# Kernel optimization log

Measured on AMD Instinct MI355X. Metric: run time of the kernel, lower is better.

The kernel has to match this reference:

```python
import jax, jax.numpy as jnp
import numpy as np

B = 16          # events per minibatch
P = 4096        # generated points per event
Q = 4096        # ground-truth points per event
SPATIAL_SIZE = 256.0


def setup_inputs() -> dict:
    key = jax.random.key(0)
    k1, k2 = jax.random.split(key)
    points_gen = jax.random.normal(k1, (B * P, 3), dtype=jnp.float32)
    # batch ids: contiguous equal-size segments per event
    batch_gen = (jnp.arange(B * P, dtype=jnp.int32) // P).astype(jnp.int32)
    # label: col 0 = batch id, cols 1:4 = coords in [0, 256), col 4 = class label
    coords = jax.random.uniform(k2, (B * Q, 3), dtype=jnp.float32) * SPATIAL_SIZE
    batch_gt = (jnp.arange(B * Q, dtype=jnp.float32) // Q)
    cls = jnp.zeros((B * Q,), dtype=jnp.float32)
    label = jnp.concatenate([batch_gt[:, None], coords, cls[:, None]], axis=1)
    return {"points_gen": points_gen, "batch_gen": batch_gen, "label": label}


def _chamfer(x, y):
    # x: [P,3], y: [Q,3] -> symmetric Chamfer distance (squared Euclidean)
    x2 = jnp.sum(x * x, axis=-1)                      # [P]
    y2 = jnp.sum(y * y, axis=-1)                      # [Q]
    d = x2[:, None] + y2[None, :] - 2.0 * (x @ y.T)   # [P,Q]
    return jnp.mean(jnp.min(d, axis=1)) + jnp.mean(jnp.min(d, axis=0))


def reference(points_gen, batch_gen, label):
    half = SPATIAL_SIZE / 2.0
    points_gt = (label[:, 1:4] - half) / half          # normalize GT to [-1,1]
    # batch ids are contiguous equal segments -> masking == reshape
    x = points_gen.reshape(B, P, 3)
    y = points_gt.reshape(B, Q, 3)
    losses = jax.vmap(_chamfer)(x, y)                  # [B]
    loss = jnp.sum(losses) / B                         # loss / count
    return loss
```

## Files before the change

kernel.cpp:

```cpp
#include <hip/hip_runtime.h>


#define NB 16
#define NP 4096
#define THREADS 256
#define INV128 0.0078125f
#define FINF __int_as_float(0x7F800000)

typedef __attribute__((ext_vector_type(8)))  short bf16x8;
typedef __attribute__((ext_vector_type(16))) float f32x16;

__device__ __forceinline__ short bf16rne(float f) {
    unsigned u = __float_as_uint(f);
    return (short)((u + 0x7FFFu + ((u >> 16) & 1u)) >> 16);
}
__device__ __forceinline__ float bf2f(short s) {
    return __uint_as_float(((unsigned)(unsigned short)s) << 16);
}

__global__ __launch_bounds__(THREADS) void chamfer_kernel(const float* __restrict__ gen,
                                                          const float* __restrict__ label,
                                                          float* __restrict__ partial) {
    __shared__ short spack[NP * 8 + 1024];
    __shared__ float wpart[8];

    int bid = blockIdx.x;
    const int dir  = bid >> 9;
    const int b    = (bid >> 5) & 15;
    const int qblk = bid & 31;
    const int tid  = threadIdx.x;
    const int lane = tid & 63;
    const int wave = tid >> 6;
    const int base = b * NP;

    if (tid < 8) spack[NP * 8 + tid] = 0;

    #pragma unroll 4
    for (int k = 0; k < 16; ++k) {
        int j = tid + k * 256;
        float x, y, z;
        if (dir == 0) {
            const float* row = label + (size_t)(base + j) * 5;
            x = fmaf(row[1], INV128, -1.0f);
            y = fmaf(row[2], INV128, -1.0f);
            z = fmaf(row[3], INV128, -1.0f);
        } else {
            const float* g = gen + (size_t)(base + j) * 3;
            x = g[0]; y = g[1]; z = g[2];
        }
        float t2 = fmaf(x, x, fmaf(y, y, z * z));
        short xh = bf16rne(x), yh = bf16rne(y), zh = bf16rne(z);
        short xl = bf16rne(x - bf2f(xh));
        short yl = bf16rne(y - bf2f(yh));
        short zl = bf16rne(z - bf2f(zh));
        short th = bf16rne(t2);
        short tl = bf16rne(t2 - bf2f(th));
        bf16x8 v = {xh, yh, zh, xl, yl, zl, th, tl};
        *(bf16x8*)(spack + j * 8) = v;
    }

    const int qrow = base + qblk * 128 + wave * 32 + (lane & 31);
    float q2 = 0.0f;
    bf16x8 afrag = (bf16x8)(short)0;
    if (lane < 32) {
        float x, y, z;
        if (dir == 0) {
            const float* g = gen + (size_t)qrow * 3;
            x = g[0]; y = g[1]; z = g[2];
        } else {
            const float* row = label + (size_t)qrow * 5;
            x = fmaf(row[1], INV128, -1.0f);
            y = fmaf(row[2], INV128, -1.0f);
            z = fmaf(row[3], INV128, -1.0f);
        }
        q2 = fmaf(x, x, fmaf(y, y, z * z));
        short ax = bf16rne(-2.0f * x), ay = bf16rne(-2.0f * y), az = bf16rne(-2.0f * z);
        const short one = 0x3F80;
        bf16x8 a = {ax, ay, az, ax, ay, az, one, one};
        afrag = a;
    }
    __syncthreads();

    const short* pa = (lane < 32) ? (spack + (lane & 31) * 8)       : (spack + NP * 8);
    const short* pb = (lane < 32) ? (spack + (lane & 31) * 8 + 256) : (spack + NP * 8);
    const int step = (lane < 32) ? 512 : 0;

    float mn[16];
    #pragma unroll
    for (int r = 0; r < 16; ++r) mn[r] = FINF;
    const f32x16 zc = {};

    bf16x8 bA = *(const bf16x8*)pa;
    bf16x8 bB = *(const bf16x8*)pb;
    #pragma unroll 2
    for (int it = 0; it < 64; ++it) {
        pa += step; pb += step;
        bf16x8 nA = *(const bf16x8*)pa;
        bf16x8 nB = *(const bf16x8*)pb;
        f32x16 ca = __builtin_amdgcn_mfma_f32_32x32x16_bf16(afrag, bA, zc, 0, 0, 0);
        f32x16 cb = __builtin_amdgcn_mfma_f32_32x32x16_bf16(afrag, bB, zc, 0, 0, 0);
        #pragma unroll
        for (int r = 0; r < 16; ++r)
            asm("v_min3_f32 %0, %1, %2, %0" : "+v"(mn[r]) : "v"(ca[r]), "v"(cb[r]));
        bA = nA; bB = nB;
    }

    #pragma unroll
    for (int m = 1; m <= 16; m <<= 1) {
        #pragma unroll
        for (int r = 0; r < 16; ++r)
            mn[r] = fminf(mn[r], __shfl_xor(mn[r], m, 64));
    }

    float s = 0.0f;
    const int h4 = (lane >> 5) * 4;
    #pragma unroll
    for (int r = 0; r < 16; ++r) {
        int row = (r & 3) + 8 * (r >> 2) + h4;
        s += mn[r] + __shfl(q2, row, 64);
    }
    if ((lane & 31) == 0) wpart[wave * 2 + (lane >> 5)] = s;
    __syncthreads();
    if (tid == 0) {
        float t = 0.0f;
        #pragma unroll
        for (int i = 0; i < 8; ++i) t += wpart[i];
        partial[blockIdx.x] = t;
    }
}

__global__ __launch_bounds__(256) void reduce_kernel(const float* __restrict__ partial,
                                                     float* __restrict__ out) {
    int i = threadIdx.x;
    float s = (partial[i] + partial[i + 256]) + (partial[i + 512] + partial[i + 768]);
    #pragma unroll
    for (int off = 32; off > 0; off >>= 1) s += __shfl_down(s, off, 64);
    __shared__ float ws4[4];
    if ((i & 63) == 0) ws4[i >> 6] = s;
    __syncthreads();
    if (i == 0) out[0] = ((ws4[0] + ws4[1]) + (ws4[2] + ws4[3])) * (1.0f / 65536.0f);
}

extern "C" void kernel_launch(void* const* d_in, const int* in_sizes, int n_in,
                              void* d_out, int out_size, void* d_ws, size_t ws_size,
                              hipStream_t stream) {
    const float* gen   = (const float*)d_in[0];
    const float* label = (const float*)d_in[2];
    float* partial = (float*)d_ws;
    float* out = (float*)d_out;

    chamfer_kernel<<<1024, THREADS, 0, stream>>>(gen, label, partial);
    reduce_kernel<<<1, 256, 0, stream>>>(partial, out);
}
```

Baseline: 100.1 us.

## Process two query blocks per workgroup to reuse staged LDS target set

Halves the grid so each workgroup stages the packed bf16 target set into LDS once and then sweeps two 128-row query blocks over it, amortising the global load and conversion cost. The inner loop now issues four MFMAs per iteration with two min3 ops per row, giving more independent work per step. The trade-off is half as many workgroups (512 on a 256-CU part) and the two query blocks run one after the other, so latency hiding and occupancy per CU may suffer.

Result: faster. 89.84 us (-10.3%).

```diff
diff --git a/kernel.cpp b/kernel.cpp
--- a/kernel.cpp
+++ b/kernel.cpp
@@ -21,17 +21,17 @@
 __global__ __launch_bounds__(THREADS) void chamfer_kernel(const float* __restrict__ gen,
                                                           const float* __restrict__ label,
                                                           float* __restrict__ partial) {
-    __shared__ short spack[NP * 8 + 1024];
+    __shared__ short spack[NP * 8 + 1280];
     __shared__ float wpart[8];
 
-    int bid = blockIdx.x;
-    const int dir  = bid >> 9;
-    const int b    = (bid >> 5) & 15;
-    const int qblk = bid & 31;
-    const int tid  = threadIdx.x;
-    const int lane = tid & 63;
-    const int wave = tid >> 6;
-    const int base = b * NP;
+    const int bid   = blockIdx.x;
+    const int dir   = bid >> 8;
+    const int b     = (bid >> 4) & 15;
+    const int qpair = bid & 15;
+    const int tid   = threadIdx.x;
+    const int lane  = tid & 63;
+    const int wave  = tid >> 6;
+    const int base  = b * NP;
 
     if (tid < 8) spack[NP * 8 + tid] = 0;
 
@@ -58,81 +58,99 @@
         bf16x8 v = {xh, yh, zh, xl, yl, zl, th, tl};
         *(bf16x8*)(spack + j * 8) = v;
     }
-
-    const int qrow = base + qblk * 128 + wave * 32 + (lane & 31);
-    float q2 = 0.0f;
-    bf16x8 afrag = (bf16x8)(short)0;
-    if (lane < 32) {
-        float x, y, z;
-        if (dir == 0) {
-            const float* g = gen + (size_t)qrow * 3;
-            x = g[0]; y = g[1]; z = g[2];
-        } else {
-            const float* row = label + (size_t)qrow * 5;
-            x = fmaf(row[1], INV128, -1.0f);
-            y = fmaf(row[2], INV128, -1.0f);
-            z = fmaf(row[3], INV128, -1.0f);
-        }
-        q2 = fmaf(x, x, fmaf(y, y, z * z));
-        short ax = bf16rne(-2.0f * x), ay = bf16rne(-2.0f * y), az = bf16rne(-2.0f * z);
-        const short one = 0x3F80;
-        bf16x8 a = {ax, ay, az, ax, ay, az, one, one};
-        afrag = a;
-    }
     __syncthreads();
 
-    const short* pa = (lane < 32) ? (spack + (lane & 31) * 8)       : (spack + NP * 8);
-    const short* pb = (lane < 32) ? (spack + (lane & 31) * 8 + 256) : (spack + NP * 8);
-    const int step = (lane < 32) ? 512 : 0;
-
-    float mn[16];
-    #pragma unroll
-    for (int r = 0; r < 16; ++r) mn[r] = FINF;
+    float sacc = 0.0f;
     const f32x16 zc = {};
 
-    bf16x8 bA = *(const bf16x8*)pa;
-    bf16x8 bB = *(const bf16x8*)pb;
-    #pragma unroll 2
-    for (int it = 0; it < 64; ++it) {
-        pa += step; pb += step;
-        bf16x8 nA = *(const bf16x8*)pa;
-        bf16x8 nB = *(const bf16x8*)pb;
-        f32x16 ca = __builtin_amdgcn_mfma_f32_32x32x16_bf16(afrag, bA, zc, 0, 0, 0);
-        f32x16 cb = __builtin_amdgcn_mfma_f32_32x32x16_bf16(afrag, bB, zc, 0, 0, 0);
+    #pragma unroll 1
+    for (int sub = 0; sub < 2; ++sub) {
+        const int qblk = qpair * 2 + sub;
+
+        const int qrow = base + qblk * 128 + wave * 32 + (lane & 31);
+        float q2 = 0.0f;
+        bf16x8 afrag = (bf16x8)(short)0;
+        if (lane < 32) {
+            float x, y, z;
+            if (dir == 0) {
+                const float* g = gen + (size_t)qrow * 3;
+                x = g[0]; y = g[1]; z = g[2];
+            } else {
+                const float* row = label + (size_t)qrow * 5;
+                x = fmaf(row[1], INV128, -1.0f);
+                y = fmaf(row[2], INV128, -1.0f);
+                z = fmaf(row[3], INV128, -1.0f);
+            }
+            q2 = fmaf(x, x, fmaf(y, y, z * z));
+            short ax = bf16rne(-2.0f * x), ay = bf16rne(-2.0f * y), az = bf16rne(-2.0f * z);
+            const short one = 0x3F80;
+            bf16x8 a = {ax, ay, az, ax, ay, az, one, one};
+            afrag = a;
+        }
+
+        float mn[16];
         #pragma unroll
-        for (int r = 0; r < 16; ++r)
-            asm("v_min3_f32 %0, %1, %2, %0" : "+v"(mn[r]) : "v"(ca[r]), "v"(cb[r]));
-        bA = nA; bB = nB;
+        for (int r = 0; r < 16; ++r) mn[r] = FINF;
+
+        const short* zl = spack + NP * 8;
+        const short* p0 = (lane < 32) ? (spack + (lane & 31) * 8)       : zl;
+        const short* p1 = (lane < 32) ? (spack + (lane & 31) * 8 + 256) : zl;
+        const short* p2 = (lane < 32) ? (spack + (lane & 31) * 8 + 512) : zl;
+        const short* p3 = (lane < 32) ? (spack + (lane & 31) * 8 + 768) : zl;
+        const int step = (lane < 32) ? 1024 : 0;
+
+        bf16x8 b0 = *(const bf16x8*)p0;
+        bf16x8 b1 = *(const bf16x8*)p1;
+        bf16x8 b2 = *(const bf16x8*)p2;
+        bf16x8 b3 = *(const bf16x8*)p3;
+        #pragma unroll 2
+        for (int it = 0; it < 32; ++it) {
+            p0 += step; p1 += step; p2 += step; p3 += step;
+            bf16x8 n0 = *(const bf16x8*)p0;
+            bf16x8 n1 = *(const bf16x8*)p1;
+            bf16x8 n2 = *(const bf16x8*)p2;
+            bf16x8 n3 = *(const bf16x8*)p3;
+            f32x16 c0 = __builtin_amdgcn_mfma_f32_32x32x16_bf16(afrag, b0, zc, 0, 0, 0);
+            f32x16 c1 = __builtin_amdgcn_mfma_f32_32x32x16_bf16(afrag, b1, zc, 0, 0, 0);
+            f32x16 c2 = __builtin_amdgcn_mfma_f32_32x32x16_bf16(afrag, b2, zc, 0, 0, 0);
+            f32x16 c3 = __builtin_amdgcn_mfma_f32_32x32x16_bf16(afrag, b3, zc, 0, 0, 0);
+            #pragma unroll
+            for (int r = 0; r < 16; ++r) {
+                asm("v_min3_f32 %0, %1, %2, %0" : "+v"(mn[r]) : "v"(c0[r]), "v"(c1[r]));
+                asm("v_min3_f32 %0, %1, %2, %0" : "+v"(mn[r]) : "v"(c2[r]), "v"(c3[r]));
+            }
+            b0 = n0; b1 = n1; b2 = n2; b3 = n3;
+        }
+
+        #pragma unroll
+        for (int m = 1; m <= 16; m <<= 1) {
+            #pragma unroll
+            for (int r = 0; r < 16; ++r)
+                mn[r] = fminf(mn[r], __shfl_xor(mn[r], m, 64));
+        }
+
+        const int h4 = (lane >> 5) * 4;
+        #pragma unroll
+        for (int r = 0; r < 16; ++r) {
+            int row = (r & 3) + 8 * (r >> 2) + h4;
+            sacc += mn[r] + __shfl(q2, row, 64);
+        }
     }
 
-    #pragma unroll
-    for (int m = 1; m <= 16; m <<= 1) {
-        #pragma unroll
-        for (int r = 0; r < 16; ++r)
-            mn[r] = fminf(mn[r], __shfl_xor(mn[r], m, 64));
-    }
-
-    float s = 0.0f;
-    const int h4 = (lane >> 5) * 4;
-    #pragma unroll
-    for (int r = 0; r < 16; ++r) {
-        int row = (r & 3) + 8 * (r >> 2) + h4;
-        s += mn[r] + __shfl(q2, row, 64);
-    }
-    if ((lane & 31) == 0) wpart[wave * 2 + (lane >> 5)] = s;
+    if ((lane & 31) == 0) wpart[wave * 2 + (lane >> 5)] = sacc;
     __syncthreads();
     if (tid == 0) {
         float t = 0.0f;
         #pragma unroll
         for (int i = 0; i < 8; ++i) t += wpart[i];
-        partial[blockIdx.x] = t;
+        partial[bid] = t;
     }
 }
 
 __global__ __launch_bounds__(256) void reduce_kernel(const float* __restrict__ partial,
                                                      float* __restrict__ out) {
     int i = threadIdx.x;
-    float s = (partial[i] + partial[i + 256]) + (partial[i + 512] + partial[i + 768]);
+    float s = partial[i] + partial[i + 256];
     #pragma unroll
     for (int off = 32; off > 0; off >>= 1) s += __shfl_down(s, off, 64);
     __shared__ float ws4[4];
@@ -149,6 +167,6 @@
     float* partial = (float*)d_ws;
     float* out = (float*)d_out;
 
-    chamfer_kernel<<<1024, THREADS, 0, stream>>>(gen, label, partial);
+    chamfer_kernel<<<512, THREADS, 0, stream>>>(gen, label, partial);
     reduce_kernel<<<1, 256, 0, stream>>>(partial, out);
 }
```
